# Kernel tuning notes

Measured on AMD Instinct MI355X. Metric: run time of the kernel, lower is better.

Reference implementation:

```python
import jax, jax.numpy as jnp
import numpy as np

B, S, E, H = 2, 2048, 1024, 8
DH = E // H          # v head dim = 128
F = DH // 2          # q/k sub-head dim = 64


def setup_inputs() -> dict:
    key = jax.random.key(0)
    ks = jax.random.split(key, 7)
    sc = E ** -0.5
    return {
        "x": jax.random.normal(ks[0], (B, S, E), dtype=jnp.float32),
        "Wq": jax.random.normal(ks[1], (E, E), dtype=jnp.float32) * sc,
        "Wk": jax.random.normal(ks[2], (E, E), dtype=jnp.float32) * sc,
        "Wv": jax.random.normal(ks[3], (E, E), dtype=jnp.float32) * sc,
        "norm_w": jnp.ones((H, DH), dtype=jnp.float32),
        "Wo": jax.random.normal(ks[4], (E, E), dtype=jnp.float32) * sc,
        "bo": jnp.zeros((E,), dtype=jnp.float32),
        "diff_weight": jnp.float32(0.2),
    }


def reference(x, Wq, Wk, Wv, norm_w, Wo, bo, diff_weight):
    b, s, e = x.shape
    # projections (Linear with weight [out,in] -> x @ W.T)
    qs = (x @ Wq.T).reshape(b, s, H, 2, F)
    ks_ = (x @ Wk.T).reshape(b, s, H, 2, F)
    vs = (x @ Wv.T).reshape(b, s, H, DH)
    scale = F ** -0.5
    # two attention branches: [2, b, h, q, k]
    scores = jnp.einsum('bqhif,bkhif->ibhqk', qs, ks_) * scale
    atts = jax.nn.softmax(scores, axis=-1)
    att = atts[0] - diff_weight * atts[1]          # [b,h,q,k]
    o = jnp.einsum('bhqk,bkhe->bqhe', att, vs)     # [b,q,h,dh]
    # RMSNorm over the joint (heads, head_dim) dims, as in nn.RMSNorm([H, DH])
    eps = jnp.finfo(o.dtype).eps
    rms = jax.lax.rsqrt(jnp.mean(o * o, axis=(-2, -1), keepdims=True) + eps)
    normed = (o * rms * norm_w).reshape(b, s, e)
    return (normed @ Wo.T + bo) * (1.0 - diff_weight)
```

## Files before the change

kernel.cpp:

```cpp
#include <hip/hip_runtime.h>
#include <hip/hip_bf16.h>
#include <math.h>


#define SDIM 2048
#define EDIM 1024
#define HDIM 8
#define DHDIM 128

typedef unsigned short u16;
typedef __attribute__((ext_vector_type(8))) short bf16x8;
typedef __attribute__((ext_vector_type(4))) short bf16x4;
typedef __attribute__((ext_vector_type(4))) u16 u16x4;
typedef __attribute__((ext_vector_type(8))) u16 u16x8;
typedef __attribute__((ext_vector_type(4))) float f32x4;

__device__ __forceinline__ u16 bf16rne(float f) {
    unsigned int u = __float_as_uint(f);
    u += 0x7fff + ((u >> 16) & 1);
    return (u16)(u >> 16);
}

__device__ __forceinline__ void gload16(void* lds, const void* g) {
    __builtin_amdgcn_global_load_lds(
        (const __attribute__((address_space(1))) unsigned int*)g,
        (__attribute__((address_space(3))) unsigned int*)lds, 16, 0, 0);
}

constexpr int GM = 4096, GN = 1024, GK = 1024;

__global__ __launch_bounds__(256) void cast_bf16(
    const float* __restrict__ x,  const float* __restrict__ wq,
    const float* __restrict__ wk, const float* __restrict__ wv,
    const float* __restrict__ wo,
    u16* __restrict__ xb,  u16* __restrict__ wqb, u16* __restrict__ wkb,
    u16* __restrict__ wvb, u16* __restrict__ wob)
{
    int bid = blockIdx.x;
    const float* src; u16* dst; int lb;
    if (bid < 2048)      { src = x;  dst = xb;  lb = bid; }
    else if (bid < 2560) { src = wq; dst = wqb; lb = bid - 2048; }
    else if (bid < 3072) { src = wk; dst = wkb; lb = bid - 2560; }
    else if (bid < 3584) { src = wv; dst = wvb; lb = bid - 3072; }
    else                 { src = wo; dst = wob; lb = bid - 3584; }
    size_t i = ((size_t)lb * 256 + threadIdx.x) * 8;
    float4 a = *(const float4*)&src[i];
    float4 b = *(const float4*)&src[i + 4];
    u16x8 o;
    o[0] = bf16rne(a.x); o[1] = bf16rne(a.y); o[2] = bf16rne(a.z); o[3] = bf16rne(a.w);
    o[4] = bf16rne(b.x); o[5] = bf16rne(b.y); o[6] = bf16rne(b.z); o[7] = bf16rne(b.w);
    *(u16x8*)&dst[i] = o;
}

struct GemmCore {
    f32x4 acc[4][4];
    int m0, n0, wm, wn, ln, quad;
};

__device__ __forceinline__ void gemm_core(
    GemmCore& g, const u16* __restrict__ A, const u16* __restrict__ W,
    u16* AsBase, u16* BsBase)
{
    const int tid = threadIdx.x;
    const int lane = tid & 63;
    const int wv = tid >> 6;
    g.ln = lane & 15; g.quad = lane >> 4;
    g.wm = (wv >> 1) * 64; g.wn = (wv & 1) * 64;
    g.m0 = blockIdx.y * 128; g.n0 = blockIdx.x * 128;

#pragma unroll
    for (int i = 0; i < 4; ++i)
#pragma unroll
        for (int j = 0; j < 4; ++j)
            g.acc[i][j] = (f32x4){0.f, 0.f, 0.f, 0.f};

    const int s0 = tid, s1 = tid + 256;
    const int ar0 = s0 >> 2, ac0 = (((s0 & 3) ^ ((ar0 >> 1) & 3)) * 8);
    const int ar1 = s1 >> 2, ac1 = (((s1 & 3) ^ ((ar1 >> 1) & 3)) * 8);
    const u16* pa0 = A + (size_t)(g.m0 + ar0) * GK + ac0;
    const u16* pa1 = A + (size_t)(g.m0 + ar1) * GK + ac1;
    const u16* pb0 = W + (size_t)(g.n0 + ar0) * GK + ac0;
    const u16* pb1 = W + (size_t)(g.n0 + ar1) * GK + ac1;
    u16* la0 = AsBase + s0 * 8; u16* la1 = AsBase + s1 * 8;
    u16* lb0 = BsBase + s0 * 8; u16* lb1 = BsBase + s1 * 8;

    const int roff = ((g.quad ^ ((g.ln >> 1) & 3)) * 8);

    for (int k0 = 0; k0 < GK; k0 += 32) {
        gload16(la0, pa0 + k0);
        gload16(la1, pa1 + k0);
        gload16(lb0, pb0 + k0);
        gload16(lb1, pb1 + k0);
        __syncthreads();

        bf16x8 af[4], bfr[4];
#pragma unroll
        for (int t = 0; t < 4; ++t) {
            af[t]  = *(const bf16x8*)&AsBase[(g.wm + t * 16 + g.ln) * 32 + roff];
            bfr[t] = *(const bf16x8*)&BsBase[(g.wn + t * 16 + g.ln) * 32 + roff];
        }
#pragma unroll
        for (int i = 0; i < 4; ++i)
#pragma unroll
            for (int j = 0; j < 4; ++j)
                g.acc[i][j] = __builtin_amdgcn_mfma_f32_16x16x32_bf16(
                    af[i], bfr[j], g.acc[i][j], 0, 0, 0);
        __syncthreads();
    }
}

__global__ __launch_bounds__(256) void gemm_qkv(
    const u16* __restrict__ A,
    const u16* __restrict__ W0, const u16* __restrict__ W1, const u16* __restrict__ W2,
    u16* __restrict__ Qb, u16* __restrict__ Kb, u16* __restrict__ Vtb)
{
    __shared__ u16 As[128 * 32];
    __shared__ u16 Bs[128 * 32];
    const int z = blockIdx.z;
    const u16* W = (z == 0) ? W0 : ((z == 1) ? W1 : W2);
    GemmCore g;
    gemm_core(g, A, W, As, Bs);

    if (z < 2) {
        const float scl = (z == 0) ? 0.125f * 1.44269504f : 1.0f;
        u16* C = (z == 0) ? Qb : Kb;
#pragma unroll
        for (int i = 0; i < 4; ++i) {
            int rb = g.m0 + g.wm + i * 16 + g.quad * 4;
#pragma unroll
            for (int r = 0; r < 4; ++r) {
                u16* crow = C + (size_t)(rb + r) * GN + g.n0 + g.wn + g.ln;
#pragma unroll
                for (int j = 0; j < 4; ++j)
                    crow[j * 16] = bf16rne(g.acc[i][j][r] * scl);
            }
        }
    } else {
        const int bb = g.m0 >> 11;
        const int sb = (g.m0 & 2047) + g.wm + g.quad * 4;
#pragma unroll
        for (int j = 0; j < 4; ++j) {
            int dhg = g.n0 + g.wn + j * 16 + g.ln;
            int hh = dhg >> 7, dh = dhg & 127;
            u16* vrow = Vtb + ((size_t)(bb * 8 + hh) * DHDIM + dh) * SDIM + sb;
#pragma unroll
            for (int i = 0; i < 4; ++i) {
                u16x4 pk;
#pragma unroll
                for (int r = 0; r < 4; ++r) pk[r] = bf16rne(g.acc[i][j][r]);
                *(u16x4*)&vrow[i * 16] = pk;
            }
        }
    }
}

__global__ __launch_bounds__(256) void gemm_out(
    const u16* __restrict__ A, const u16* __restrict__ W,
    float* __restrict__ C, const float* __restrict__ bias,
    const float* __restrict__ dwp)
{
    __shared__ u16 As[128 * 32];
    __shared__ u16 Bs[128 * 32];
    GemmCore g;
    gemm_core(g, A, W, As, Bs);

    const float scale = 1.0f - dwp[0];
    float bv[4];
#pragma unroll
    for (int j = 0; j < 4; ++j) bv[j] = bias[g.n0 + g.wn + j * 16 + g.ln];
#pragma unroll
    for (int i = 0; i < 4; ++i) {
        int rb = g.m0 + g.wm + i * 16 + g.quad * 4;
#pragma unroll
        for (int r = 0; r < 4; ++r) {
            float* crow = C + (size_t)(rb + r) * GN + g.n0 + g.wn + g.ln;
#pragma unroll
            for (int j = 0; j < 4; ++j)
                crow[j * 16] = (g.acc[i][j][r] + bv[j]) * scale;
        }
    }
}

#define KBUF 4096
#define VBUF 8192

__global__ __launch_bounds__(256, 2) void attn_mfma(
    const u16* __restrict__ Qb, const u16* __restrict__ Kb,
    const u16* __restrict__ Vtb,
    float* __restrict__ Oacc, float* __restrict__ Lacc)
{
    __shared__ u16 Ks[2 * KBUF];
    __shared__ u16 Vs[2 * VBUF];

    const int tid = threadIdx.x;
    const int wv   = tid >> 6;
    const int lane = tid & 63;
    const int ln = lane & 15, quad = lane >> 4;
    const int lx = ln & 7;
    const int vkey = (ln >> 1) & 3;
    const int bh = blockIdx.y, b = bh >> 3, h = bh & 7;
    const int q0 = blockIdx.x * 128 + wv * 32;
    const int BR = blockIdx.z;

    const size_t qoff = (size_t)b * SDIM * EDIM + h * DHDIM + BR * 64;
    bf16x8 aq[2][2];
#pragma unroll
    for (int qt = 0; qt < 2; ++qt) {
        const u16* qp = Qb + qoff + (size_t)(q0 + qt * 16 + ln) * EDIM + quad * 8;
        aq[qt][0] = *(const bf16x8*)(qp);
        aq[qt][1] = *(const bf16x8*)(qp + 32);
    }

    const int s0 = tid, s1 = tid + 256;
    const int kr0 = s0 >> 3, kc0 = ((s0 & 7) ^ (kr0 & 7)) * 8;
    const int kr1 = s1 >> 3, kc1 = ((s1 & 7) ^ (kr1 & 7)) * 8;
    const u16* kg0 = Kb + (size_t)(b * SDIM + kr0) * EDIM + h * DHDIM + BR * 64 + kc0;
    const u16* kg1 = Kb + (size_t)(b * SDIM + kr1) * EDIM + h * DHDIM + BR * 64 + kc1;
    const int vr0 = s0 >> 2, vc0 = ((s0 & 3) ^ ((vr0 >> 1) & 3)) * 8;
    const int vr1 = s1 >> 2, vc1 = ((s1 & 3) ^ ((vr1 >> 1) & 3)) * 8;
    const u16* vg0 = Vtb + ((size_t)bh * DHDIM + vr0) * SDIM + vc0;
    const u16* vg1 = Vtb + ((size_t)bh * DHDIM + vr1) * SDIM + vc1;
    u16* ksd0 = Ks + s0 * 8; u16* ksd1 = Ks + s1 * 8;
    u16* vsd0 = Vs + s0 * 8; u16* vsd1 = Vs + s1 * 8;

    gload16(ksd0, kg0); gload16(ksd1, kg1);
    gload16(vsd0, vg0); gload16(vsd1, vg1);
    gload16(vsd0 + 4096, vg0 + 32); gload16(vsd1 + 4096, vg1 + 32);
    kg0 += 64 * EDIM; kg1 += 64 * EDIM; vg0 += 64; vg1 += 64;

    f32x4 acc[2][8];
#pragma unroll
    for (int qt = 0; qt < 2; ++qt)
#pragma unroll
        for (int d = 0; d < 8; ++d)
            acc[qt][d] = (f32x4){0.f, 0.f, 0.f, 0.f};
    float lsum[2] = {0.f, 0.f};
    const f32x4 z4 = (f32x4){0.f, 0.f, 0.f, 0.f};

    for (int it = 0; it < 32; ++it) {
        const int cur = it & 1;
        __syncthreads();

        if (it < 31) {
            const int kb = (cur ^ 1) * KBUF, vb2 = (cur ^ 1) * VBUF;
            gload16(ksd0 + kb, kg0); gload16(ksd1 + kb, kg1);
            gload16(vsd0 + vb2, vg0); gload16(vsd1 + vb2, vg1);
            gload16(vsd0 + vb2 + 4096, vg0 + 32); gload16(vsd1 + vb2 + 4096, vg1 + 32);
            kg0 += 64 * EDIM; kg1 += 64 * EDIM; vg0 += 64; vg1 += 64;
        }

        const u16* Kc = Ks + cur * KBUF;
        const u16* Vc = Vs + cur * VBUF;

        bf16x8 kf[4][2];
#pragma unroll
        for (int t2 = 0; t2 < 4; ++t2) {
            const int rb = (t2 * 16 + ln) * 64;
            kf[t2][0] = *(const bf16x8*)&Kc[rb + ((quad ^ lx) * 8)];
            kf[t2][1] = *(const bf16x8*)&Kc[rb + (((4 + quad) ^ lx) * 8)];
        }

        f32x4 st[2][4];
#pragma unroll
        for (int t2 = 0; t2 < 4; ++t2)
#pragma unroll
            for (int qt = 0; qt < 2; ++qt) {
                f32x4 s = __builtin_amdgcn_mfma_f32_16x16x32_bf16(kf[t2][0], aq[qt][0], z4, 0, 0, 0);
                st[qt][t2] = __builtin_amdgcn_mfma_f32_16x16x32_bf16(kf[t2][1], aq[qt][1], s, 0, 0, 0);
            }

        bf16x8 vf[8][2];
#pragma unroll
        for (int dt = 0; dt < 8; ++dt) {
            const int vb = (dt * 16 + ln) * 32;
#pragma unroll
            for (int ks = 0; ks < 2; ++ks) {
                const u16* Vk = Vc + ks * 4096;
                bf16x4 vlo = *(const bf16x4*)&Vk[vb + ((((quad >> 1) + 0) ^ vkey) * 8 + (quad & 1) * 4)];
                bf16x4 vhi = *(const bf16x4*)&Vk[vb + ((((quad >> 1) + 2) ^ vkey) * 8 + (quad & 1) * 4)];
                vf[dt][ks] = __builtin_shufflevector(vlo, vhi, 0, 1, 2, 3, 4, 5, 6, 7);
            }
        }

        union { unsigned int u[4]; bf16x8 v; } ap[2][2];
#pragma unroll
        for (int qt = 0; qt < 2; ++qt)
#pragma unroll
            for (int ks = 0; ks < 2; ++ks) {
                float e0 = exp2f(st[qt][2 * ks][0]), e1 = exp2f(st[qt][2 * ks][1]);
                float e2 = exp2f(st[qt][2 * ks][2]), e3 = exp2f(st[qt][2 * ks][3]);
                float f0 = exp2f(st[qt][2 * ks + 1][0]), f1 = exp2f(st[qt][2 * ks + 1][1]);
                float f2 = exp2f(st[qt][2 * ks + 1][2]), f3 = exp2f(st[qt][2 * ks + 1][3]);
                lsum[qt] += (e0 + e1) + (e2 + e3) + (f0 + f1) + (f2 + f3);
                ap[qt][ks].u[0] = __builtin_amdgcn_perm(__float_as_uint(e1), __float_as_uint(e0), 0x07060302u);
                ap[qt][ks].u[1] = __builtin_amdgcn_perm(__float_as_uint(e3), __float_as_uint(e2), 0x07060302u);
                ap[qt][ks].u[2] = __builtin_amdgcn_perm(__float_as_uint(f1), __float_as_uint(f0), 0x07060302u);
                ap[qt][ks].u[3] = __builtin_amdgcn_perm(__float_as_uint(f3), __float_as_uint(f2), 0x07060302u);
            }

#pragma unroll
        for (int dt = 0; dt < 8; ++dt)
#pragma unroll
            for (int ks = 0; ks < 2; ++ks)
#pragma unroll
                for (int qt = 0; qt < 2; ++qt)
                    acc[qt][dt] = __builtin_amdgcn_mfma_f32_16x16x32_bf16(ap[qt][ks].v, vf[dt][ks], acc[qt][dt], 0, 0, 0);
    }

#pragma unroll
    for (int qt = 0; qt < 2; ++qt) {
#pragma unroll
        for (int r = 0; r < 4; ++r) {
            size_t row = (size_t)(b * SDIM + q0 + qt * 16 + quad * 4 + r);
            float* o = Oacc + ((row * 8 + h) * 2 + BR) * 128 + ln;
#pragma unroll
            for (int dt = 0; dt < 8; ++dt)
                o[dt * 16] = acc[qt][dt][r];
        }
    }
#pragma unroll
    for (int qt = 0; qt < 2; ++qt) {
        float l = lsum[qt];
        l += __shfl_xor(l, 16, 64); l += __shfl_xor(l, 32, 64);
        if (quad == 0)
            Lacc[(size_t)((b * 8 + h) * 2 + BR) * SDIM + q0 + qt * 16 + ln] = l;
    }
}

__global__ __launch_bounds__(256) void rms_combine(
    const float* __restrict__ Oacc, const float* __restrict__ Lacc,
    const float* __restrict__ nw, u16* __restrict__ Nb,
    const float* __restrict__ dwp)
{
    const int row = blockIdx.x;
    const int tid = threadIdx.x;
    const int h = tid >> 5, dh0 = (tid & 31) * 4;
    const int b = row >> 11, q = row & 2047;

    size_t ob = ((size_t)row * 8 + h) * 2 * 128;
    f32x4 a0 = *(const f32x4*)&Oacc[ob + dh0];
    f32x4 a1 = *(const f32x4*)&Oacc[ob + 128 + dh0];
    float l0 = Lacc[(size_t)((b * 8 + h) * 2 + 0) * SDIM + q];
    float l1 = Lacc[(size_t)((b * 8 + h) * 2 + 1) * SDIM + q];
    const float dw = dwp[0];
    float inv0 = 1.0f / l0;
    float inv1 = dw / l1;
    float o[4];
#pragma unroll
    for (int k = 0; k < 4; ++k) o[k] = a0[k] * inv0 - a1[k] * inv1;

    float ss = o[0] * o[0] + o[1] * o[1] + o[2] * o[2] + o[3] * o[3];
    ss += __shfl_xor(ss, 1,  64);
    ss += __shfl_xor(ss, 2,  64);
    ss += __shfl_xor(ss, 4,  64);
    ss += __shfl_xor(ss, 8,  64);
    ss += __shfl_xor(ss, 16, 64);
    ss += __shfl_xor(ss, 32, 64);
    __shared__ float red[4];
    if ((tid & 63) == 0) red[tid >> 6] = ss;
    __syncthreads();
    float tot = red[0] + red[1] + red[2] + red[3];
    float rms = rsqrtf(tot * (1.0f / 1024.0f) + 1.1920929e-07f);

    float4 w = *(const float4*)&nw[tid * 4];
    u16x4 pk;
    pk[0] = bf16rne(o[0] * rms * w.x);
    pk[1] = bf16rne(o[1] * rms * w.y);
    pk[2] = bf16rne(o[2] * rms * w.z);
    pk[3] = bf16rne(o[3] * rms * w.w);
    *(u16x4*)&Nb[(size_t)row * EDIM + tid * 4] = pk;
}

extern "C" void kernel_launch(void* const* d_in, const int* in_sizes, int n_in,
                              void* d_out, int out_size, void* d_ws, size_t ws_size,
                              hipStream_t stream)
{
    const float* x   = (const float*)d_in[0];
    const float* Wq  = (const float*)d_in[1];
    const float* Wk  = (const float*)d_in[2];
    const float* Wv  = (const float*)d_in[3];
    const float* nw  = (const float*)d_in[4];
    const float* Wo  = (const float*)d_in[5];
    const float* bo  = (const float*)d_in[6];
    const float* dwp = (const float*)d_in[7];
    float* out = (float*)d_out;

    float* Oacc = (float*)d_ws;
    u16*  xb   = (u16*)d_ws;
    u16*  wob  = (u16*)((char*)d_ws + 33554432);
    u16*  wqb  = wob + 1048576;
    u16*  wkb  = wqb + 1048576;
    u16*  wvb  = wkb + 1048576;
    float* Lacc = (float*)wqb;
    u16*  Qb   = wvb + 1048576;
    u16*  Kb   = Qb + 4194304;
    u16*  Vtb  = Kb + 4194304;
    u16*  Nb   = Qb;

    cast_bf16<<<4096, 256, 0, stream>>>(x, Wq, Wk, Wv, Wo,
                                        xb, wqb, wkb, wvb, wob);
    gemm_qkv<<<dim3(GN / 128, GM / 128, 3), 256, 0, stream>>>(
        xb, wqb, wkb, wvb, Qb, Kb, Vtb);
    attn_mfma<<<dim3(SDIM / 128, 2 * HDIM, 2), 256, 0, stream>>>(
        Qb, Kb, Vtb, Oacc, Lacc);
    rms_combine<<<4096, 256, 0, stream>>>(Oacc, Lacc, nw, Nb, dwp);
    gemm_out<<<dim3(GN / 128, GM / 128, 1), 256, 0, stream>>>(
        Nb, wob, out, bo, dwp);
}
```

Before: 238.7 us.

## Double GEMM K-tile to 64 with 8-way swizzle and raise priority around attention MFMAs

The shared GEMM core now stages a 64-wide K slice per iteration instead of 32. This halves the number of loop iterations and barrier pairs, and it uses a new 8-chunk XOR swizzle to keep LDS reads conflict-free. LDS per block doubles to 32 KB, which may reduce occupancy. Separately, the attention kernel wraps its QK and PV MFMA blocks in s_setprio raises so that waves in the matrix phase get issue priority over waves doing exp and loads.

```diff
diff --git a/kernel.cpp b/kernel.cpp
--- a/kernel.cpp
+++ b/kernel.cpp
@@ -74,37 +74,50 @@
         for (int j = 0; j < 4; ++j)
             g.acc[i][j] = (f32x4){0.f, 0.f, 0.f, 0.f};
 
-    const int s0 = tid, s1 = tid + 256;
-    const int ar0 = s0 >> 2, ac0 = (((s0 & 3) ^ ((ar0 >> 1) & 3)) * 8);
-    const int ar1 = s1 >> 2, ac1 = (((s1 & 3) ^ ((ar1 >> 1) & 3)) * 8);
+    const int s0 = tid, s1 = tid + 256, s2 = tid + 512, s3 = tid + 768;
+    const int ar0 = s0 >> 3, ac0 = ((s0 & 7) ^ (ar0 & 7)) * 8;
+    const int ar1 = s1 >> 3, ac1 = ((s1 & 7) ^ (ar1 & 7)) * 8;
+    const int ar2 = s2 >> 3, ac2 = ((s2 & 7) ^ (ar2 & 7)) * 8;
+    const int ar3 = s3 >> 3, ac3 = ((s3 & 7) ^ (ar3 & 7)) * 8;
     const u16* pa0 = A + (size_t)(g.m0 + ar0) * GK + ac0;
     const u16* pa1 = A + (size_t)(g.m0 + ar1) * GK + ac1;
+    const u16* pa2 = A + (size_t)(g.m0 + ar2) * GK + ac2;
+    const u16* pa3 = A + (size_t)(g.m0 + ar3) * GK + ac3;
     const u16* pb0 = W + (size_t)(g.n0 + ar0) * GK + ac0;
     const u16* pb1 = W + (size_t)(g.n0 + ar1) * GK + ac1;
+    const u16* pb2 = W + (size_t)(g.n0 + ar2) * GK + ac2;
+    const u16* pb3 = W + (size_t)(g.n0 + ar3) * GK + ac3;
     u16* la0 = AsBase + s0 * 8; u16* la1 = AsBase + s1 * 8;
+    u16* la2 = AsBase + s2 * 8; u16* la3 = AsBase + s3 * 8;
     u16* lb0 = BsBase + s0 * 8; u16* lb1 = BsBase + s1 * 8;
-
-    const int roff = ((g.quad ^ ((g.ln >> 1) & 3)) * 8);
-
-    for (int k0 = 0; k0 < GK; k0 += 32) {
-        gload16(la0, pa0 + k0);
-        gload16(la1, pa1 + k0);
-        gload16(lb0, pb0 + k0);
-        gload16(lb1, pb1 + k0);
+    u16* lb2 = BsBase + s2 * 8; u16* lb3 = BsBase + s3 * 8;
+
+    for (int k0 = 0; k0 < GK; k0 += 64) {
+        gload16(la0, pa0 + k0); gload16(la1, pa1 + k0);
+        gload16(la2, pa2 + k0); gload16(la3, pa3 + k0);
+        gload16(lb0, pb0 + k0); gload16(lb1, pb1 + k0);
+        gload16(lb2, pb2 + k0); gload16(lb3, pb3 + k0);
         __syncthreads();
 
-        bf16x8 af[4], bfr[4];
+        bf16x8 af[4][2], bfr[4][2];
 #pragma unroll
         for (int t = 0; t < 4; ++t) {
-            af[t]  = *(const bf16x8*)&AsBase[(g.wm + t * 16 + g.ln) * 32 + roff];
-            bfr[t] = *(const bf16x8*)&BsBase[(g.wn + t * 16 + g.ln) * 32 + roff];
+#pragma unroll
+            for (int kk = 0; kk < 2; ++kk) {
+                const int ra = g.wm + t * 16 + g.ln;
+                const int rb = g.wn + t * 16 + g.ln;
+                af[t][kk]  = *(const bf16x8*)&AsBase[ra * 64 + (((kk * 4 + g.quad) ^ (ra & 7)) * 8)];
+                bfr[t][kk] = *(const bf16x8*)&BsBase[rb * 64 + (((kk * 4 + g.quad) ^ (rb & 7)) * 8)];
+            }
         }
 #pragma unroll
         for (int i = 0; i < 4; ++i)
 #pragma unroll
             for (int j = 0; j < 4; ++j)
-                g.acc[i][j] = __builtin_amdgcn_mfma_f32_16x16x32_bf16(
-                    af[i], bfr[j], g.acc[i][j], 0, 0, 0);
+#pragma unroll
+                for (int kk = 0; kk < 2; ++kk)
+                    g.acc[i][j] = __builtin_amdgcn_mfma_f32_16x16x32_bf16(
+                        af[i][kk], bfr[j][kk], g.acc[i][j], 0, 0, 0);
         __syncthreads();
     }
 }
@@ -114,8 +127,8 @@
     const u16* __restrict__ W0, const u16* __restrict__ W1, const u16* __restrict__ W2,
     u16* __restrict__ Qb, u16* __restrict__ Kb, u16* __restrict__ Vtb)
 {
-    __shared__ u16 As[128 * 32];
-    __shared__ u16 Bs[128 * 32];
+    __shared__ u16 As[128 * 64];
+    __shared__ u16 Bs[128 * 64];
     const int z = blockIdx.z;
     const u16* W = (z == 0) ? W0 : ((z == 1) ? W1 : W2);
     GemmCore g;
@@ -159,8 +172,8 @@
     float* __restrict__ C, const float* __restrict__ bias,
     const float* __restrict__ dwp)
 {
-    __shared__ u16 As[128 * 32];
-    __shared__ u16 Bs[128 * 32];
+    __shared__ u16 As[128 * 64];
+    __shared__ u16 Bs[128 * 64];
     GemmCore g;
     gemm_core(g, A, W, As, Bs);
 
@@ -261,6 +274,7 @@
         }
 
         f32x4 st[2][4];
+        __builtin_amdgcn_s_setprio(1);
 #pragma unroll
         for (int t2 = 0; t2 < 4; ++t2)
 #pragma unroll
@@ -268,6 +282,7 @@
                 f32x4 s = __builtin_amdgcn_mfma_f32_16x16x32_bf16(kf[t2][0], aq[qt][0], z4, 0, 0, 0);
                 st[qt][t2] = __builtin_amdgcn_mfma_f32_16x16x32_bf16(kf[t2][1], aq[qt][1], s, 0, 0, 0);
             }
+        __builtin_amdgcn_s_setprio(0);
 
         bf16x8 vf[8][2];
 #pragma unroll
@@ -298,6 +313,7 @@
                 ap[qt][ks].u[3] = __builtin_amdgcn_perm(__float_as_uint(f3), __float_as_uint(f2), 0x07060302u);
             }
 
+        __builtin_amdgcn_s_setprio(1);
 #pragma unroll
         for (int dt = 0; dt < 8; ++dt)
 #pragma unroll
@@ -305,6 +321,7 @@
 #pragma unroll
                 for (int qt = 0; qt < 2; ++qt)
                     acc[qt][dt] = __builtin_amdgcn_mfma_f32_16x16x32_bf16(ap[qt][ks].v, vf[dt][ks], acc[qt][dt], 0, 0, 0);
+        __builtin_amdgcn_s_setprio(0);
     }
 
 #pragma unroll
```

New measurement: 241.8 us. Within noise of the previous version (+1.3%).
